# Performance work log

Measured on AMD Instinct MI355X. Metric: run time of the kernel, lower is better.

Reference implementation:

```python
import jax, jax.numpy as jnp
import numpy as np

MAX_SET_SIZE = 32  # f1_query_max_set_size


def setup_inputs() -> dict:
    key = jax.random.key(0)
    k1, k2, k3, k4 = jax.random.split(key, 4)
    B, Lq, L, d_qk, d_v = 8, 512, 4096, 64, 64
    q = jax.random.normal(k1, (B, Lq, d_qk), dtype=jnp.float32)
    k = jax.random.normal(k2, (B, L, d_qk), dtype=jnp.float32)
    v = jax.random.normal(k3, (B, L, d_v), dtype=jnp.float32)
    mask = jax.random.randint(k4, (B * Lq, L), 0, 2).astype(bool)
    return {"q": q, "k": k, "v": v, "mask": mask}


def _query_conditioned_subset_pool(rank_scores, v, batch_idx, mask, max_set_size):
    # rank_scores/mask: [N, L]; v: [B, L, d_v]
    N, L = rank_scores.shape
    keep = min(max_set_size, L)
    neg_inf = jnp.finfo(rank_scores.dtype).min
    masked_scores = jnp.where(mask, rank_scores.astype(jnp.float32), neg_inf)
    _, top_idx = jax.lax.top_k(masked_scores, keep)          # [N, keep]
    picked = jnp.take_along_axis(mask, top_idx, axis=1)
    sortable = jnp.where(picked, top_idx, L)                 # sentinel L for unpicked
    sortable = jnp.sort(sortable, axis=1)                    # restore index order
    picked = sortable < L
    safe_idx = jnp.where(picked, sortable, 0)                # [N, keep]
    sel_v = v[batch_idx[:, None], safe_idx]                  # [N, keep, d_v]
    sel_scores = jnp.take_along_axis(rank_scores, safe_idx, axis=1)
    sel_scores = jnp.where(picked, sel_scores, neg_inf)
    attn = jax.nn.softmax(sel_scores, axis=1)
    non_empty = picked.any(axis=1, keepdims=True)
    attn = jnp.where(picked & non_empty, attn, jnp.zeros_like(attn))
    return jnp.einsum('nk,nkd->nd', attn.astype(sel_v.dtype), sel_v)


def reference(q, k, v, mask):
    B, Lq, d_qk = q.shape
    L = k.shape[1]
    d_v = v.shape[-1]
    scale = 1.0 / float(np.sqrt(d_qk))
    # rank_scores [B, Lq, L] -> flat chains [B*Lq, L]
    rank_scores = jnp.einsum('bqd,bld->bql', q, k) * scale
    rs_flat = rank_scores.reshape(B * Lq, L)
    batch_idx = jnp.repeat(jnp.arange(B), Lq)
    # f1 = mean over masked support: sum_v / clamp(count, 1)
    mask_f = mask.astype(q.dtype)                            # [B*Lq, L]
    count = jnp.clip(mask_f.sum(axis=1), 1.0, None)          # [B*Lq]
    sum_v = jnp.einsum('bql,bld->bqd', mask_f.reshape(B, Lq, L), v).reshape(B * Lq, d_v)
    mean_out = sum_v / count[:, None]
    # f1_query_mode='add': query-conditioned restricted pooling over top-k subset
    q_ctx = _query_conditioned_subset_pool(rs_flat, v, batch_idx, mask, MAX_SET_SIZE)
    out = mean_out + q_ctx
    return out.reshape(B, Lq, d_v)
```

## Files before the change

kernel.cpp:

```cpp
#include <hip/hip_runtime.h>
#include <float.h>
#include <math.h>

#define LQ   512
#define LL   4096
#define DD   64
#define KEEP 32
#define NB   8
#define NROWS (NB * LQ)

#define RT    32
#define NLC   8
#define LC    (LL / NLC)
#define LSP   128
#define NPAIR (LC / LSP)

#define WS_VT    (NROWS * LL)
#define WS_TOTAL (WS_VT + (NB * DD * LL) / 2)

#define MASKED_KEY 0x00800000u

typedef short  bf16x8 __attribute__((ext_vector_type(8)));
typedef float  f32x4  __attribute__((ext_vector_type(4)));

__device__ __forceinline__ float dot4(float4 a, float4 b) {
    return a.x * b.x + a.y * b.y + a.z * b.z + a.w * b.w;
}
__device__ __forceinline__ unsigned short f2bf(float f) {
    unsigned int u = __float_as_uint(f);
    return (unsigned short)((u + 0x7FFFu + ((u >> 16) & 1u)) >> 16);
}

#define TP_LB 256
__global__ __launch_bounds__(256) void k_vt(
    const float* __restrict__ v, unsigned short* __restrict__ vt)
{
    __shared__ unsigned short tile[DD][TP_LB + 8];
    const int t  = threadIdx.x;
    const int b  = blockIdx.x >> 4;
    const int l0 = (blockIdx.x & 15) * TP_LB;

    const float4* vg = reinterpret_cast<const float4*>(v + ((size_t)b * LL + l0) * DD);
    #pragma unroll
    for (int i = 0; i < 16; ++i) {
        int j = t + 256 * i;
        float4 f = vg[j];
        int l = j >> 4, dq = (j & 15) * 4;
        tile[dq + 0][l] = f2bf(f.x);
        tile[dq + 1][l] = f2bf(f.y);
        tile[dq + 2][l] = f2bf(f.z);
        tile[dq + 3][l] = f2bf(f.w);
    }
    __syncthreads();
    const int d = t >> 2, seg = t & 3;
    const uint4* src = reinterpret_cast<const uint4*>(&tile[d][seg * 64]);
    uint4* dst = reinterpret_cast<uint4*>(vt + ((size_t)b * DD + d) * LL + l0 + seg * 64);
    #pragma unroll
    for (int i = 0; i < 8; ++i) dst[i] = src[i];
}

__global__ __launch_bounds__(256) void k_mean(
    const int* __restrict__ mask,
    const unsigned short* __restrict__ vt,
    float* __restrict__ out)
{
    __shared__ float sums[4][4][16][16];
    __shared__ float cnt_s[4][16];

    const int t     = threadIdx.x;
    const int wave  = t >> 6;
    const int lane  = t & 63;
    const int n0    = blockIdx.x * 16;
    const int b     = n0 / LQ;
    const int row_a = lane & 15;
    const int chunk = lane >> 4;

    const int* mrow = mask + (size_t)(n0 + row_a) * LL + wave * 1024 + chunk * 8;
    const unsigned short* vbase = vt + (size_t)b * DD * LL + wave * 1024 + chunk * 8;

    f32x4 acc[4];
    #pragma unroll
    for (int dt = 0; dt < 4; ++dt) acc[dt] = (f32x4){0.f, 0.f, 0.f, 0.f};
    int cnt = 0;

    for (int l0 = 0; l0 < 1024; l0 += 32) {
        int4 ma = *reinterpret_cast<const int4*>(mrow + l0);
        int4 mb = *reinterpret_cast<const int4*>(mrow + l0 + 4);
        cnt += (ma.x != 0) + (ma.y != 0) + (ma.z != 0) + (ma.w != 0)
             + (mb.x != 0) + (mb.y != 0) + (mb.z != 0) + (mb.w != 0);
        unsigned int p[4];
        p[0] = (ma.x ? 0x3F80u : 0u) | (ma.y ? 0x3F800000u : 0u);
        p[1] = (ma.z ? 0x3F80u : 0u) | (ma.w ? 0x3F800000u : 0u);
        p[2] = (mb.x ? 0x3F80u : 0u) | (mb.y ? 0x3F800000u : 0u);
        p[3] = (mb.z ? 0x3F80u : 0u) | (mb.w ? 0x3F800000u : 0u);
        bf16x8 afrag = *reinterpret_cast<bf16x8*>(p);
        #pragma unroll
        for (int dt = 0; dt < 4; ++dt) {
            bf16x8 bfrag = *reinterpret_cast<const bf16x8*>(
                vbase + (size_t)(dt * 16 + row_a) * LL + l0);
            acc[dt] = __builtin_amdgcn_mfma_f32_16x16x32_bf16(afrag, bfrag, acc[dt], 0, 0, 0);
        }
    }
    cnt += __shfl_xor(cnt, 16);
    cnt += __shfl_xor(cnt, 32);
    if (lane < 16) cnt_s[wave][lane] = (float)cnt;
    #pragma unroll
    for (int dt = 0; dt < 4; ++dt)
        #pragma unroll
        for (int r = 0; r < 4; ++r)
            sums[wave][dt][chunk * 4 + r][row_a] = acc[dt][r];
    __syncthreads();

    const int d = t & 63, rgrp = t >> 6;
    #pragma unroll
    for (int rr = 0; rr < 4; ++rr) {
        const int row = rgrp * 4 + rr;
        float s = sums[0][d >> 4][row][d & 15] + sums[1][d >> 4][row][d & 15]
                + sums[2][d >> 4][row][d & 15] + sums[3][d >> 4][row][d & 15];
        float c = cnt_s[0][row] + cnt_s[1][row] + cnt_s[2][row] + cnt_s[3][row];
        if (c < 1.f) c = 1.f;
        out[(size_t)(n0 + row) * DD + d] = s / c;
    }
}

__global__ __launch_bounds__(256)
__attribute__((amdgpu_waves_per_eu(2, 4)))
void k_scores(
    const float* __restrict__ q,
    const float* __restrict__ kmat,
    const int*   __restrict__ mask,
    float*       __restrict__ ws_sc)
{
    __shared__ float4 Ss4[16 * LSP];

    const int t    = threadIdx.x;
    const int wave = t >> 6;
    const int lane = t & 63;
    const int rt   = blockIdx.x >> 3;
    const int lc   = blockIdx.x & (NLC - 1);
    const int n0   = rt * RT;
    const int b    = n0 / LQ;
    const int lbase = lc * LC;

    int qbase[8];
    #pragma unroll
    for (int p = 0; p < 8; ++p)
        qbase[p] = __builtin_amdgcn_readfirstlane((n0 + wave * 8 + p) * DD);

    const float4* kg = reinterpret_cast<const float4*>(kmat) + (size_t)b * LL * 16;

    for (int s = 0; s < NPAIR; ++s) {
        const int l0 = lbase + s * LSP;
        __syncthreads();
        #pragma unroll
        for (int i = 0; i < 2; ++i)
            #pragma unroll
            for (int j = 0; j < 4; ++j)
                Ss4[(wave * 4 + j) * LSP + lane + 64 * i] =
                    kg[(size_t)(l0 + lane + 64 * i) * 16 + wave * 4 + j];
        __syncthreads();

        float acc0[8], acc1[8];
        #pragma unroll
        for (int p = 0; p < 8; ++p) { acc0[p] = 0.f; acc1[p] = 0.f; }
        #pragma unroll
        for (int dc = 0; dc < 16; ++dc) {
            float4 ka = Ss4[dc * LSP + lane];
            float4 kb = Ss4[dc * LSP + 64 + lane];
            #pragma unroll
            for (int p = 0; p < 8; ++p) {
                float4 q4 = *reinterpret_cast<const float4*>(q + qbase[p] + dc * 4);
                acc0[p] += dot4(ka, q4);
                acc1[p] += dot4(kb, q4);
            }
        }
        #pragma unroll
        for (int p = 0; p < 8; ++p) {
            const int r = wave * 8 + p;
            int m0 = mask[(size_t)(n0 + r) * LL + l0 + lane];
            int m1 = mask[(size_t)(n0 + r) * LL + l0 + 64 + lane];
            ws_sc[(size_t)(n0 + r) * LL + l0 + lane]      = m0 ? acc0[p] * 0.125f : -FLT_MAX;
            ws_sc[(size_t)(n0 + r) * LL + l0 + 64 + lane] = m1 ? acc1[p] * 0.125f : -FLT_MAX;
        }
    }
}

__global__ __launch_bounds__(256, 3) void k_select(
    const float* __restrict__ vmat,
    const float* __restrict__ ws,
    float*       __restrict__ out)
{
    __shared__ unsigned int hist[4][256];
    __shared__ unsigned int selKey[4][KEEP];
    __shared__ int          selIdx[4][KEEP];
    __shared__ float        wsel[4][KEEP];
    __shared__ int          selCnt[4], eqCnt[4];

    const int t    = threadIdx.x;
    const int wave = t >> 6;
    const int lane = t & 63;
    const int row  = blockIdx.x * 4 + wave;
    const int b    = row / LQ;

    float o = out[(size_t)row * DD + lane];

    unsigned int key[64];
    {
        const float4* sg = reinterpret_cast<const float4*>(ws) + (size_t)row * (LL / 4);
        #pragma unroll
        for (int i = 0; i < 16; ++i) {
            float4 f = sg[lane + 64 * i];
            float vals[4] = { f.x, f.y, f.z, f.w };
            #pragma unroll
            for (int c = 0; c < 4; ++c) {
                unsigned int u = __float_as_uint(vals[c]);
                key[4 * i + c] = ((int)u < 0) ? ~u : (u | 0x80000000u);
            }
        }
    }

    unsigned int prefix = 0, quota = KEEP;
    #pragma unroll
    for (int pass = 0; pass < 4; ++pass) {
        const int shift = 24 - 8 * pass;
        const unsigned int hs = (pass == 0) ? 0u : (unsigned int)(32 - 8 * pass);
        reinterpret_cast<uint4*>(hist[wave])[lane] = make_uint4(0u, 0u, 0u, 0u);
        __asm__ volatile("s_waitcnt lgkmcnt(0)" ::: "memory");
        #pragma unroll
        for (int e = 0; e < 64; ++e) {
            bool act = (pass == 0) || ((key[e] >> hs) == prefix);
            if (act) atomicAdd(&hist[wave][(key[e] >> shift) & 255u], 1u);
        }
        __asm__ volatile("s_waitcnt lgkmcnt(0)" ::: "memory");
        uint4 h = reinterpret_cast<const uint4*>(hist[wave])[lane];
        unsigned int s4  = h.x + h.y + h.z + h.w;
        unsigned int suf = s4;
        #pragma unroll
        for (int off = 1; off < 64; off <<= 1) {
            unsigned int v = (unsigned int)__shfl_down((int)suf, off);
            if (lane + off < 64) suf += v;
        }
        unsigned int above = suf - s4;
        bool cond = (suf >= quota) && (above < quota);
        unsigned int Bq = 0, nq = 0;
        if (cond) {
            unsigned int hb[4] = { h.x, h.y, h.z, h.w };
            unsigned int run = above;
            int Bj = 0;
            #pragma unroll
            for (int j = 3; j >= 0; --j) {
                unsigned int nb = run + hb[j];
                if (nb >= quota) { Bj = j; break; }
                run = nb;
            }
            Bq = (unsigned int)(lane * 4 + Bj);
            nq = quota - run;
        }
        unsigned long long bal = __ballot(cond);
        int src = __ffsll(bal) - 1;
        Bq = (unsigned int)__shfl((int)Bq, src);
        nq = (unsigned int)__shfl((int)nq, src);
        prefix = (prefix << 8) | Bq;
        quota  = nq;
    }
    const unsigned int T = prefix;
    const bool take_eq = (T != MASKED_KEY);

    if (lane < KEEP) { wsel[wave][lane] = 0.f; selIdx[wave][lane] = 0; }
    if (lane == 0)   { selCnt[wave] = 0; eqCnt[wave] = 0; }
    __asm__ volatile("s_waitcnt lgkmcnt(0)" ::: "memory");
    #pragma unroll
    for (int e = 0; e < 64; ++e) {
        unsigned int k = key[e];
        if (k > T) {
            int slot = atomicAdd(&selCnt[wave], 1);
            selKey[wave][slot] = k;
            selIdx[wave][slot] = 256 * (e >> 2) + 4 * lane + (e & 3);
        } else if (take_eq && k == T) {
            int t2 = atomicAdd(&eqCnt[wave], 1);
            if (t2 < (int)quota) {
                int slot = atomicAdd(&selCnt[wave], 1);
                selKey[wave][slot] = k;
                selIdx[wave][slot] = 256 * (e >> 2) + 4 * lane + (e & 3);
            }
        }
    }
    __asm__ volatile("s_waitcnt lgkmcnt(0)" ::: "memory");
    const int S = selCnt[wave];

    if (S > 0) {
        float vj = -FLT_MAX;
        if (lane < S) {
            unsigned int kk = selKey[wave][lane];
            unsigned int u = (kk & 0x80000000u) ? (kk ^ 0x80000000u) : ~kk;
            vj = __uint_as_float(u);
        }
        float mx = vj;
        #pragma unroll
        for (int off = 1; off < 64; off <<= 1) mx = fmaxf(mx, __shfl_xor(mx, off));
        float e = (lane < S) ? expf(vj - mx) : 0.f;
        float sum = e;
        #pragma unroll
        for (int off = 1; off < 64; off <<= 1) sum += __shfl_xor(sum, off);
        if (lane < S) wsel[wave][lane] = e / sum;
        __asm__ volatile("s_waitcnt lgkmcnt(0)" ::: "memory");
        const float* vb = vmat + (size_t)b * LL * DD + lane;
        #pragma unroll
        for (int j = 0; j < KEEP; ++j) {
            float wj = wsel[wave][j];
            int   ij = selIdx[wave][j];
            o += wj * vb[(size_t)ij * DD];
        }
    }
    out[(size_t)row * DD + lane] = o;
}

#define QT   2
#define NT   256
#define NTILES (LL / NT)

__global__ __launch_bounds__(NT, 4) void ga_fused_fb(
    const float* __restrict__ q, const float* __restrict__ kmat,
    const float* __restrict__ vmat, const int* __restrict__ mask,
    float* __restrict__ out)
{
    __shared__ float sc[QT][LL];
    __shared__ float q_s[QT][DD];
    __shared__ unsigned long long mbits[QT][LL / 64];
    __shared__ float redv[4][QT][DD];
    __shared__ float mean_s[QT][DD];
    __shared__ int   count_s[QT];
    __shared__ int   sel_idx[QT][KEEP];
    __shared__ float sel_val[QT][KEEP];
    __shared__ int   sel_cnt[QT];
    __shared__ float wred[4];
    __shared__ int   ired[4];
    __shared__ int   brk;
    __shared__ float wgt[QT][KEEP];

    const int t = threadIdx.x, wave = t >> 6, lane = t & 63;
    const int n0 = blockIdx.x * QT, b = n0 / LQ;

    if (t < QT) sel_cnt[t] = 0;
    if (t < QT * DD) q_s[t >> 6][t & 63] = q[(size_t)(n0 + (t >> 6)) * DD + (t & 63)];
    __syncthreads();

    const float4* q4_0 = reinterpret_cast<const float4*>(&q_s[0][0]);
    const float4* q4_1 = reinterpret_cast<const float4*>(&q_s[1][0]);
    for (int tile = 0; tile < NTILES; ++tile) {
        int l = tile * NT + t;
        const float4* kr = reinterpret_cast<const float4*>(kmat + (size_t)(b * LL + l) * DD);
        float d0 = 0.f, d1 = 0.f;
        #pragma unroll
        for (int i = 0; i < 16; ++i) {
            float4 kk = kr[i], qa = q4_0[i], qb = q4_1[i];
            d0 += kk.x * qa.x + kk.y * qa.y + kk.z * qa.z + kk.w * qa.w;
            d1 += kk.x * qb.x + kk.y * qb.y + kk.z * qb.z + kk.w * qb.w;
        }
        int mv0 = mask[(size_t)n0 * LL + l];
        int mv1 = mask[(size_t)(n0 + 1) * LL + l];
        unsigned long long b0 = __ballot(mv0 != 0);
        unsigned long long b1 = __ballot(mv1 != 0);
        if (lane == 0) { mbits[0][tile * 4 + wave] = b0; mbits[1][tile * 4 + wave] = b1; }
        sc[0][l] = mv0 ? d0 * 0.125f : -FLT_MAX;
        sc[1][l] = mv1 ? d1 * 0.125f : -FLT_MAX;
    }
    __syncthreads();

    if (wave < QT) {
        int c = (int)__popcll(mbits[wave][lane]);
        for (int off = 32; off >= 1; off >>= 1) c += __shfl_down(c, off);
        if (lane == 0) count_s[wave] = c;
    }
    {
        float acc0 = 0.f, acc1 = 0.f;
        const int g = wave, d = lane;
        for (int wi = 0; wi < LL / 64; ++wi) {
            unsigned long long w0 = mbits[0][wi], w1 = mbits[1][wi];
            const float* vp = vmat + (size_t)(b * LL + wi * 64 + g) * DD + d;
            #pragma unroll 4
            for (int ii = 0; ii < 16; ++ii) {
                int sh = g + 4 * ii;
                float vv = vp[(size_t)(4 * ii) * DD];
                if ((w0 >> sh) & 1ULL) acc0 += vv;
                if ((w1 >> sh) & 1ULL) acc1 += vv;
            }
        }
        redv[g][0][d] = acc0; redv[g][1][d] = acc1;
    }
    __syncthreads();
    if (t < QT * DD) {
        int qt = t >> 6, dd = t & 63;
        float s2 = redv[0][qt][dd] + redv[1][qt][dd] + redv[2][qt][dd] + redv[3][qt][dd];
        int c = count_s[qt]; if (c < 1) c = 1;
        mean_s[qt][dd] = s2 / (float)c;
    }
    __syncthreads();

    for (int qt = 0; qt < QT; ++qt) {
        for (int s = 0; s < KEEP; ++s) {
            float m = -FLT_MAX; int mi = LL;
            for (int j = 0; j < NTILES; ++j) {
                int l = j * NT + t;
                float val = sc[qt][l];
                if (val > m) { m = val; mi = l; }
            }
            for (int off = 32; off >= 1; off >>= 1) {
                float ov = __shfl_down(m, off);
                int   oi = __shfl_down(mi, off);
                if (ov > m || (ov == m && oi < mi)) { m = ov; mi = oi; }
            }
            if (lane == 0) { wred[wave] = m; ired[wave] = mi; }
            __syncthreads();
            if (t == 0) {
                float bv = wred[0]; int bi = ired[0];
                for (int w2 = 1; w2 < 4; ++w2) {
                    float ov = wred[w2]; int oi = ired[w2];
                    if (ov > bv || (ov == bv && oi < bi)) { bv = ov; bi = oi; }
                }
                if (bv > -FLT_MAX) {
                    sel_idx[qt][s] = bi; sel_val[qt][s] = bv; sel_cnt[qt] = s + 1;
                    sc[qt][bi] = -FLT_MAX; brk = 0;
                } else brk = 1;
            }
            __syncthreads();
            if (brk) break;
        }
    }

    if (wave < QT) {
        int qt = wave, S = sel_cnt[qt];
        if (S > 0) {
            float mx = sel_val[qt][0];
            float e = 0.f;
            if (lane < S) e = expf(sel_val[qt][lane] - mx);
            float ssum = e;
            for (int off = 32; off >= 1; off >>= 1) ssum += __shfl_xor(ssum, off);
            if (lane < S) wgt[qt][lane] = e / ssum;
        }
    }
    __syncthreads();
    if (wave < QT) {
        int qt = wave, S = sel_cnt[qt];
        float o = mean_s[qt][lane];
        for (int j = 0; j < S; ++j)
            o += wgt[qt][j] * vmat[(size_t)(b * LL + sel_idx[qt][j]) * DD + lane];
        out[(size_t)(n0 + qt) * DD + lane] = o;
    }
}

extern "C" void kernel_launch(void* const* d_in, const int* in_sizes, int n_in,
                              void* d_out, int out_size, void* d_ws, size_t ws_size,
                              hipStream_t stream) {
    const float* q    = (const float*)d_in[0];
    const float* kmat = (const float*)d_in[1];
    const float* vmat = (const float*)d_in[2];
    const int*   mask = (const int*)d_in[3];
    float* out = (float*)d_out;

    const size_t need = (size_t)WS_TOTAL * sizeof(float);
    if (ws_size >= need) {
        float* ws = (float*)d_ws;
        unsigned short* vt = (unsigned short*)(ws + WS_VT);
        hipLaunchKernelGGL(k_scores, dim3((NROWS / RT) * NLC), dim3(256), 0, stream,
                           q, kmat, mask, ws);
        hipLaunchKernelGGL(k_vt, dim3(NB * 16), dim3(256), 0, stream, vmat, vt);
        hipLaunchKernelGGL(k_mean, dim3(NROWS / 16), dim3(256), 0, stream,
                           mask, vt, out);
        hipLaunchKernelGGL(k_select, dim3(NROWS / 4), dim3(256), 0, stream,
                           vmat, ws, out);
    } else {
        hipLaunchKernelGGL(ga_fused_fb, dim3(NROWS / QT), dim3(NT), 0, stream,
                           q, kmat, vmat, mask, out);
    }
}
```

Baseline: 290.1 us.

## Fuse per-chunk top-k into score kernel and pass bitmask to mean kernel

The score kernel no longer writes the full masked score matrix to workspace. Each block runs a radix select over its 512-column chunk and emits 32 candidate keys and indices per row, plus the row mask packed as a bitmask. The merge kernel then selects the final top-32 from 256 candidates per row, and the mean kernel reads the packed bits instead of the int32 mask. This removes large global writes and re-reads, at the cost of a heavier, register-hungry score kernel (keys[8][8], occupancy hint lowered) and a serial per-row select loop.

Measured after the change: 389.7 us. +34.3%, slower.

```diff
diff --git a/kernel.cpp b/kernel.cpp
--- a/kernel.cpp
+++ b/kernel.cpp
@@ -14,8 +14,12 @@
 #define LC    (LL / NLC)
 #define LSP   128
 #define NPAIR (LC / LSP)
-
-#define WS_VT    (NROWS * LL)
+#define NCAND (NLC * KEEP)
+
+#define WS_CKEY  0
+#define WS_CIDX  (NROWS * NCAND)
+#define WS_BM    (2 * NROWS * NCAND)
+#define WS_VT    (WS_BM + NROWS * 128)
 #define WS_TOTAL (WS_VT + (NB * DD * LL) / 2)
 
 #define MASKED_KEY 0x00800000u
@@ -29,6 +33,10 @@
 __device__ __forceinline__ unsigned short f2bf(float f) {
     unsigned int u = __float_as_uint(f);
     return (unsigned short)((u + 0x7FFFu + ((u >> 16) & 1u)) >> 16);
+}
+__device__ __forceinline__ unsigned int f2key(float f) {
+    unsigned int u = __float_as_uint(f);
+    return ((int)u < 0) ? ~u : (u | 0x80000000u);
 }
 
 #define TP_LB 256
@@ -59,77 +67,15 @@
     for (int i = 0; i < 8; ++i) dst[i] = src[i];
 }
 
-__global__ __launch_bounds__(256) void k_mean(
-    const int* __restrict__ mask,
-    const unsigned short* __restrict__ vt,
-    float* __restrict__ out)
-{
-    __shared__ float sums[4][4][16][16];
-    __shared__ float cnt_s[4][16];
-
-    const int t     = threadIdx.x;
-    const int wave  = t >> 6;
-    const int lane  = t & 63;
-    const int n0    = blockIdx.x * 16;
-    const int b     = n0 / LQ;
-    const int row_a = lane & 15;
-    const int chunk = lane >> 4;
-
-    const int* mrow = mask + (size_t)(n0 + row_a) * LL + wave * 1024 + chunk * 8;
-    const unsigned short* vbase = vt + (size_t)b * DD * LL + wave * 1024 + chunk * 8;
-
-    f32x4 acc[4];
-    #pragma unroll
-    for (int dt = 0; dt < 4; ++dt) acc[dt] = (f32x4){0.f, 0.f, 0.f, 0.f};
-    int cnt = 0;
-
-    for (int l0 = 0; l0 < 1024; l0 += 32) {
-        int4 ma = *reinterpret_cast<const int4*>(mrow + l0);
-        int4 mb = *reinterpret_cast<const int4*>(mrow + l0 + 4);
-        cnt += (ma.x != 0) + (ma.y != 0) + (ma.z != 0) + (ma.w != 0)
-             + (mb.x != 0) + (mb.y != 0) + (mb.z != 0) + (mb.w != 0);
-        unsigned int p[4];
-        p[0] = (ma.x ? 0x3F80u : 0u) | (ma.y ? 0x3F800000u : 0u);
-        p[1] = (ma.z ? 0x3F80u : 0u) | (ma.w ? 0x3F800000u : 0u);
-        p[2] = (mb.x ? 0x3F80u : 0u) | (mb.y ? 0x3F800000u : 0u);
-        p[3] = (mb.z ? 0x3F80u : 0u) | (mb.w ? 0x3F800000u : 0u);
-        bf16x8 afrag = *reinterpret_cast<bf16x8*>(p);
-        #pragma unroll
-        for (int dt = 0; dt < 4; ++dt) {
-            bf16x8 bfrag = *reinterpret_cast<const bf16x8*>(
-                vbase + (size_t)(dt * 16 + row_a) * LL + l0);
-            acc[dt] = __builtin_amdgcn_mfma_f32_16x16x32_bf16(afrag, bfrag, acc[dt], 0, 0, 0);
-        }
-    }
-    cnt += __shfl_xor(cnt, 16);
-    cnt += __shfl_xor(cnt, 32);
-    if (lane < 16) cnt_s[wave][lane] = (float)cnt;
-    #pragma unroll
-    for (int dt = 0; dt < 4; ++dt)
-        #pragma unroll
-        for (int r = 0; r < 4; ++r)
-            sums[wave][dt][chunk * 4 + r][row_a] = acc[dt][r];
-    __syncthreads();
-
-    const int d = t & 63, rgrp = t >> 6;
-    #pragma unroll
-    for (int rr = 0; rr < 4; ++rr) {
-        const int row = rgrp * 4 + rr;
-        float s = sums[0][d >> 4][row][d & 15] + sums[1][d >> 4][row][d & 15]
-                + sums[2][d >> 4][row][d & 15] + sums[3][d >> 4][row][d & 15];
-        float c = cnt_s[0][row] + cnt_s[1][row] + cnt_s[2][row] + cnt_s[3][row];
-        if (c < 1.f) c = 1.f;
-        out[(size_t)(n0 + row) * DD + d] = s / c;
-    }
-}
-
 __global__ __launch_bounds__(256)
-__attribute__((amdgpu_waves_per_eu(2, 4)))
+__attribute__((amdgpu_waves_per_eu(2, 3)))
 void k_scores(
     const float* __restrict__ q,
     const float* __restrict__ kmat,
     const int*   __restrict__ mask,
-    float*       __restrict__ ws_sc)
+    unsigned int* __restrict__ ckey,
+    unsigned int* __restrict__ cidx,
+    uint4*        __restrict__ bm)
 {
     __shared__ float4 Ss4[16 * LSP];
 
@@ -149,6 +95,8 @@
 
     const float4* kg = reinterpret_cast<const float4*>(kmat) + (size_t)b * LL * 16;
 
+    unsigned int keys[8][8];
+
     for (int s = 0; s < NPAIR; ++s) {
         const int l0 = lbase + s * LSP;
         __syncthreads();
@@ -179,22 +127,173 @@
             const int r = wave * 8 + p;
             int m0 = mask[(size_t)(n0 + r) * LL + l0 + lane];
             int m1 = mask[(size_t)(n0 + r) * LL + l0 + 64 + lane];
-            ws_sc[(size_t)(n0 + r) * LL + l0 + lane]      = m0 ? acc0[p] * 0.125f : -FLT_MAX;
-            ws_sc[(size_t)(n0 + r) * LL + l0 + 64 + lane] = m1 ? acc1[p] * 0.125f : -FLT_MAX;
-        }
-    }
-}
-
-__global__ __launch_bounds__(256, 3) void k_select(
+            unsigned long long b0 = __ballot(m0 != 0);
+            unsigned long long b1 = __ballot(m1 != 0);
+            if (lane == 0)
+                bm[(size_t)(n0 + r) * 32 + lc * 4 + s] =
+                    make_uint4((unsigned)b0, (unsigned)(b0 >> 32),
+                               (unsigned)b1, (unsigned)(b1 >> 32));
+            keys[p][s * 2]     = m0 ? f2key(acc0[p] * 0.125f) : MASKED_KEY;
+            keys[p][s * 2 + 1] = m1 ? f2key(acc1[p] * 0.125f) : MASKED_KEY;
+        }
+    }
+    __syncthreads();
+
+    unsigned int* hist = reinterpret_cast<unsigned int*>(Ss4) + wave * 256;
+
+    #pragma unroll 1
+    for (int p = 0; p < 8; ++p) {
+        const int row = n0 + wave * 8 + p;
+        unsigned int prefix = 0, quota = KEEP;
+        #pragma unroll 1
+        for (int pass = 0; pass < 4; ++pass) {
+            const int shift = 24 - 8 * pass;
+            const unsigned int hs = (pass == 0) ? 0u : (unsigned int)(32 - 8 * pass);
+            reinterpret_cast<uint4*>(hist)[lane] = make_uint4(0u, 0u, 0u, 0u);
+            __asm__ volatile("s_waitcnt lgkmcnt(0)" ::: "memory");
+            #pragma unroll
+            for (int e = 0; e < 8; ++e) {
+                unsigned int k = keys[p][e];
+                bool act = (pass == 0) || ((k >> hs) == prefix);
+                if (act) atomicAdd(&hist[(k >> shift) & 255u], 1u);
+            }
+            __asm__ volatile("s_waitcnt lgkmcnt(0)" ::: "memory");
+            uint4 h = reinterpret_cast<const uint4*>(hist)[lane];
+            unsigned int s4  = h.x + h.y + h.z + h.w;
+            unsigned int suf = s4;
+            #pragma unroll
+            for (int off = 1; off < 64; off <<= 1) {
+                unsigned int v = (unsigned int)__shfl_down((int)suf, off);
+                if (lane + off < 64) suf += v;
+            }
+            unsigned int above = suf - s4;
+            bool cond = (suf >= quota) && (above < quota);
+            unsigned int Bq = 0, nq = 0;
+            if (cond) {
+                unsigned int hb[4] = { h.x, h.y, h.z, h.w };
+                unsigned int run = above;
+                int Bj = 0;
+                #pragma unroll
+                for (int j = 3; j >= 0; --j) {
+                    unsigned int nb = run + hb[j];
+                    if (nb >= quota) { Bj = j; break; }
+                    run = nb;
+                }
+                Bq = (unsigned int)(lane * 4 + Bj);
+                nq = quota - run;
+            }
+            unsigned long long bal = __ballot(cond);
+            int src = __ffsll(bal) - 1;
+            Bq = (unsigned int)__shfl((int)Bq, src);
+            nq = (unsigned int)__shfl((int)nq, src);
+            prefix = (prefix << 8) | Bq;
+            quota  = nq;
+        }
+        const unsigned int T = prefix;
+        const bool take_eq = (T != MASKED_KEY);
+        const unsigned long long ltm = (1ull << lane) - 1ull;
+        unsigned int* ck = ckey + (size_t)row * NCAND + lc * KEEP;
+        unsigned int* ci = cidx + (size_t)row * NCAND + lc * KEEP;
+        int base = 0, eqbase = 0;
+        #pragma unroll
+        for (int e = 0; e < 8; ++e) {
+            unsigned int k = keys[p][e];
+            bool gt = k > T;
+            bool eq = take_eq && (k == T);
+            unsigned long long bgt = __ballot(gt);
+            unsigned long long beq = __ballot(eq);
+            int slot = -1;
+            if (gt) slot = base + (int)__popcll(bgt & ltm);
+            if (eq) {
+                int t2 = eqbase + (int)__popcll(beq & ltm);
+                if (t2 < (int)quota) slot = (KEEP - (int)quota) + t2;
+            }
+            base   += (int)__popcll(bgt);
+            eqbase += (int)__popcll(beq);
+            if (slot >= 0) {
+                ck[slot] = k;
+                ci[slot] = (unsigned)(lbase + (e >> 1) * 128 + (e & 1) * 64 + lane);
+            }
+        }
+        int eqt = eqbase < (int)quota ? eqbase : (int)quota;
+        int S = base + (take_eq ? eqt : 0);
+        if (lane >= S && lane < KEEP) { ck[lane] = MASKED_KEY; ci[lane] = 0u; }
+    }
+}
+
+__global__ __launch_bounds__(256) void k_mean(
+    const unsigned int* __restrict__ bm,
+    const unsigned short* __restrict__ vt,
+    float* __restrict__ out)
+{
+    __shared__ float sums[4][4][16][16];
+    __shared__ float cnt_s[4][16];
+
+    const int t     = threadIdx.x;
+    const int wave  = t >> 6;
+    const int lane  = t & 63;
+    const int n0    = blockIdx.x * 16;
+    const int b     = n0 / LQ;
+    const int row_a = lane & 15;
+    const int chunk = lane >> 4;
+
+    const unsigned int* bmrow = bm + (size_t)(n0 + row_a) * 128 + wave * 32;
+    const unsigned short* vbase = vt + (size_t)b * DD * LL + wave * 1024 + chunk * 8;
+
+    f32x4 acc[4];
+    #pragma unroll
+    for (int dt = 0; dt < 4; ++dt) acc[dt] = (f32x4){0.f, 0.f, 0.f, 0.f};
+    int cnt = 0;
+
+    for (int l0 = 0; l0 < 1024; l0 += 32) {
+        unsigned int w = bmrow[l0 >> 5];
+        unsigned int byte = (w >> (chunk * 8)) & 0xFFu;
+        cnt += __popc(byte);
+        unsigned int p[4];
+        p[0] = ((byte &   1u) ? 0x3F80u : 0u) | ((byte &   2u) ? 0x3F800000u : 0u);
+        p[1] = ((byte &   4u) ? 0x3F80u : 0u) | ((byte &   8u) ? 0x3F800000u : 0u);
+        p[2] = ((byte &  16u) ? 0x3F80u : 0u) | ((byte &  32u) ? 0x3F800000u : 0u);
+        p[3] = ((byte &  64u) ? 0x3F80u : 0u) | ((byte & 128u) ? 0x3F800000u : 0u);
+        bf16x8 afrag = *reinterpret_cast<bf16x8*>(p);
+        #pragma unroll
+        for (int dt = 0; dt < 4; ++dt) {
+            bf16x8 bfrag = *reinterpret_cast<const bf16x8*>(
+                vbase + (size_t)(dt * 16 + row_a) * LL + l0);
+            acc[dt] = __builtin_amdgcn_mfma_f32_16x16x32_bf16(afrag, bfrag, acc[dt], 0, 0, 0);
+        }
+    }
+    cnt += __shfl_xor(cnt, 16);
+    cnt += __shfl_xor(cnt, 32);
+    if (lane < 16) cnt_s[wave][lane] = (float)cnt;
+    #pragma unroll
+    for (int dt = 0; dt < 4; ++dt)
+        #pragma unroll
+        for (int r = 0; r < 4; ++r)
+            sums[wave][dt][chunk * 4 + r][row_a] = acc[dt][r];
+    __syncthreads();
+
+    const int d = t & 63, rgrp = t >> 6;
+    #pragma unroll
+    for (int rr = 0; rr < 4; ++rr) {
+        const int row = rgrp * 4 + rr;
+        float s = sums[0][d >> 4][row][d & 15] + sums[1][d >> 4][row][d & 15]
+                + sums[2][d >> 4][row][d & 15] + sums[3][d >> 4][row][d & 15];
+        float c = cnt_s[0][row] + cnt_s[1][row] + cnt_s[2][row] + cnt_s[3][row];
+        if (c < 1.f) c = 1.f;
+        out[(size_t)(n0 + row) * DD + d] = s / c;
+    }
+}
+
+__global__ __launch_bounds__(256, 3) void k_merge(
     const float* __restrict__ vmat,
-    const float* __restrict__ ws,
+    const unsigned int* __restrict__ ckey,
+    const unsigned int* __restrict__ cidx,
     float*       __restrict__ out)
 {
     __shared__ unsigned int hist[4][256];
-    __shared__ unsigned int selKey[4][KEEP];
-    __shared__ int          selIdx[4][KEEP];
+    __shared__ unsigned int selK[4][KEEP];
+    __shared__ unsigned int selI[4][KEEP];
     __shared__ float        wsel[4][KEEP];
-    __shared__ int          selCnt[4], eqCnt[4];
 
     const int t    = threadIdx.x;
     const int wave = t >> 6;
@@ -204,32 +303,23 @@
 
     float o = out[(size_t)row * DD + lane];
 
-    unsigned int key[64];
-    {
-        const float4* sg = reinterpret_cast<const float4*>(ws) + (size_t)row * (LL / 4);
-        #pragma unroll
-        for (int i = 0; i < 16; ++i) {
-            float4 f = sg[lane + 64 * i];
-            float vals[4] = { f.x, f.y, f.z, f.w };
-            #pragma unroll
-            for (int c = 0; c < 4; ++c) {
-                unsigned int u = __float_as_uint(vals[c]);
-                key[4 * i + c] = ((int)u < 0) ? ~u : (u | 0x80000000u);
-            }
-        }
-    }
+    uint4 k4 = reinterpret_cast<const uint4*>(ckey + (size_t)row * NCAND)[lane];
+    uint4 i4 = reinterpret_cast<const uint4*>(cidx + (size_t)row * NCAND)[lane];
+    unsigned int key[4] = { k4.x, k4.y, k4.z, k4.w };
+    unsigned int idx[4] = { i4.x, i4.y, i4.z, i4.w };
 
     unsigned int prefix = 0, quota = KEEP;
-    #pragma unroll
+    #pragma unroll 1
     for (int pass = 0; pass < 4; ++pass) {
         const int shift = 24 - 8 * pass;
         const unsigned int hs = (pass == 0) ? 0u : (unsigned int)(32 - 8 * pass);
         reinterpret_cast<uint4*>(hist[wave])[lane] = make_uint4(0u, 0u, 0u, 0u);
         __asm__ volatile("s_waitcnt lgkmcnt(0)" ::: "memory");
         #pragma unroll
-        for (int e = 0; e < 64; ++e) {
-            bool act = (pass == 0) || ((key[e] >> hs) == prefix);
-            if (act) atomicAdd(&hist[wave][(key[e] >> shift) & 255u], 1u);
+        for (int e = 0; e < 4; ++e) {
+            unsigned int k = key[e];
+            bool act = (pass == 0) || ((k >> hs) == prefix);
+            if (act) atomicAdd(&hist[wave][(k >> shift) & 255u], 1u);
         }
         __asm__ volatile("s_waitcnt lgkmcnt(0)" ::: "memory");
         uint4 h = reinterpret_cast<const uint4*>(hist[wave])[lane];
@@ -265,33 +355,35 @@
     }
     const unsigned int T = prefix;
     const bool take_eq = (T != MASKED_KEY);
-
-    if (lane < KEEP) { wsel[wave][lane] = 0.f; selIdx[wave][lane] = 0; }
-    if (lane == 0)   { selCnt[wave] = 0; eqCnt[wave] = 0; }
+    const unsigned long long ltm = (1ull << lane) - 1ull;
+
+    if (lane < KEEP) { wsel[wave][lane] = 0.f; selI[wave][lane] = 0u; }
+    int base = 0, eqbase = 0;
+    #pragma unroll
+    for (int e = 0; e < 4; ++e) {
+        unsigned int k = key[e];
+        bool gt = k > T;
+        bool eq = take_eq && (k == T);
+        unsigned long long bgt = __ballot(gt);
+        unsigned long long beq = __ballot(eq);
+        int slot = -1;
+        if (gt) slot = base + (int)__popcll(bgt & ltm);
+        if (eq) {
+            int t2 = eqbase + (int)__popcll(beq & ltm);
+            if (t2 < (int)quota) slot = (KEEP - (int)quota) + t2;
+        }
+        base   += (int)__popcll(bgt);
+        eqbase += (int)__popcll(beq);
+        if (slot >= 0) { selK[wave][slot] = k; selI[wave][slot] = idx[e]; }
+    }
+    int eqt = eqbase < (int)quota ? eqbase : (int)quota;
+    const int S = base + (take_eq ? eqt : 0);
     __asm__ volatile("s_waitcnt lgkmcnt(0)" ::: "memory");
-    #pragma unroll
-    for (int e = 0; e < 64; ++e) {
-        unsigned int k = key[e];
-        if (k > T) {
-            int slot = atomicAdd(&selCnt[wave], 1);
-            selKey[wave][slot] = k;
-            selIdx[wave][slot] = 256 * (e >> 2) + 4 * lane + (e & 3);
-        } else if (take_eq && k == T) {
-            int t2 = atomicAdd(&eqCnt[wave], 1);
-            if (t2 < (int)quota) {
-                int slot = atomicAdd(&selCnt[wave], 1);
-                selKey[wave][slot] = k;
-                selIdx[wave][slot] = 256 * (e >> 2) + 4 * lane + (e & 3);
-            }
-        }
-    }
-    __asm__ volatile("s_waitcnt lgkmcnt(0)" ::: "memory");
-    const int S = selCnt[wave];
 
     if (S > 0) {
         float vj = -FLT_MAX;
         if (lane < S) {
-            unsigned int kk = selKey[wave][lane];
+            unsigned int kk = selK[wave][lane];
             unsigned int u = (kk & 0x80000000u) ? (kk ^ 0x80000000u) : ~kk;
             vj = __uint_as_float(u);
         }
@@ -308,7 +400,7 @@
         #pragma unroll
         for (int j = 0; j < KEEP; ++j) {
             float wj = wsel[wave][j];
-            int   ij = selIdx[wave][j];
+            unsigned int ij = selI[wave][j];
             o += wj * vb[(size_t)ij * DD];
         }
     }
@@ -461,14 +553,17 @@
     const size_t need = (size_t)WS_TOTAL * sizeof(float);
     if (ws_size >= need) {
         float* ws = (float*)d_ws;
-        unsigned short* vt = (unsigned short*)(ws + WS_VT);
+        unsigned int*   ckey = (unsigned int*)(ws + WS_CKEY);
+        unsigned int*   cidx = (unsigned int*)(ws + WS_CIDX);
+        unsigned int*   bmw  = (unsigned int*)(ws + WS_BM);
+        unsigned short* vt   = (unsigned short*)(ws + WS_VT);
         hipLaunchKernelGGL(k_scores, dim3((NROWS / RT) * NLC), dim3(256), 0, stream,
-                           q, kmat, mask, ws);
+                           q, kmat, mask, ckey, cidx, (uint4*)bmw);
         hipLaunchKernelGGL(k_vt, dim3(NB * 16), dim3(256), 0, stream, vmat, vt);
         hipLaunchKernelGGL(k_mean, dim3(NROWS / 16), dim3(256), 0, stream,
-                           mask, vt, out);
-        hipLaunchKernelGGL(k_select, dim3(NROWS / 4), dim3(256), 0, stream,
-                           vmat, ws, out);
+                           bmw, vt, out);
+        hipLaunchKernelGGL(k_merge, dim3(NROWS / 4), dim3(256), 0, stream,
+                           vmat, ckey, cidx, out);
     } else {
         hipLaunchKernelGGL(ga_fused_fb, dim3(NROWS / QT), dim3(NT), 0, stream,
                            q, kmat, vmat, mask, out);
```
